# Performance work log

Hardware: AMD Instinct MI355X
Metric: run time of the kernel (lower is better)

Reference implementation:

```python
import jax, jax.numpy as jnp
import numpy as np

N_EMBD = 1024
HEAD_SIZE = 64
TOP_K = 32


def setup_inputs() -> dict:
    key = jax.random.key(0)
    ks = jax.random.split(key, 10)
    B, T, C, D, N = 4, 2048, N_EMBD, HEAD_SIZE, 16384
    s = 1.0 / np.sqrt(C)
    return {
        "x": jax.random.normal(ks[0], (B, T, C), jnp.float32),
        "mem_keys": jax.random.normal(ks[1], (B, N, D), jnp.float32),
        "mem_vals": jax.random.normal(ks[2], (B, N, D), jnp.float32),
        "Wq": jax.random.normal(ks[3], (C, D), jnp.float32) * s,
        "bq": jnp.zeros((D,), jnp.float32),
        "Wk": jax.random.normal(ks[4], (C, D), jnp.float32) * s,
        "bk": jnp.zeros((D,), jnp.float32),
        "Wv": jax.random.normal(ks[5], (C, D), jnp.float32) * s,
        "bv": jnp.zeros((D,), jnp.float32),
        "gate": jax.random.normal(ks[6], (1,), jnp.float32),
    }


def reference(x, mem_keys, mem_vals, Wq, bq, Wk, bk, Wv, bv, gate):
    B, T, C = x.shape
    scale = 1.0 / jnp.sqrt(jnp.asarray(C, x.dtype))  # note: scaled by n_embd, as in source
    q = x @ Wq + bq  # [B,T,D]
    k = x @ Wk + bk
    v = x @ Wv + bv
    # causal self-attention
    att = jnp.einsum("btd,bsd->bts", q, k) * scale
    causal = jnp.tril(jnp.ones((T, T), bool))
    att = jnp.where(causal[None], att, -jnp.inf)
    att = jax.nn.softmax(att, axis=-1)
    out = jnp.einsum("bts,bsd->btd", att, v)  # [B,T,D]
    # kNN memory attention: top-k inner-product search over memory bank
    scores = jnp.einsum("btd,bnd->btn", q, mem_keys)  # [B,T,N]
    _, idx = jax.lax.top_k(scores, TOP_K)  # [B,T,K]
    mem_k = jnp.take_along_axis(mem_keys[:, None], idx[..., None], axis=2)  # [B,T,K,D]
    mem_v = jnp.take_along_axis(mem_vals[:, None], idx[..., None], axis=2)  # [B,T,K,D]
    mem_att = jax.nn.softmax(jnp.einsum("btd,btkd->btk", q, mem_k) * scale, axis=-1)
    mem_out = jnp.einsum("btk,btkd->btd", mem_att, mem_v)  # [B,T,D]
    g = gate[0]
    md_out = out * g + mem_out * (1.0 - g)  # gated combine; dropout is identity at eval
    return md_out
```

## Files before the change

kernel.cpp:

```cpp
#include <hip/hip_runtime.h>
#include <math.h>

#define B_ 4
#define T_ 2048
#define C_ 1024
#define D_ 64
#define N_ 16384
#define K_ 32
#define SCALE 0.03125f
#define NEGINF -3.402823e38f

typedef __attribute__((ext_vector_type(8))) short short8_t;
typedef __attribute__((ext_vector_type(4))) float f32x4;

__device__ __forceinline__ unsigned short f2bf(float x) {
    union { float f; unsigned u; } a; a.f = x;
    const unsigned r = a.u + 0x7fffu + ((a.u >> 16) & 1u);
    return (unsigned short)(r >> 16);
}
__device__ __forceinline__ float bf2f(unsigned short h) {
    union { unsigned u; float f; } a; a.u = ((unsigned)h) << 16;
    return a.f;
}

__global__ __launch_bounds__(192) void qkv_proj_kernel(
    const float* __restrict__ x,
    const float* __restrict__ Wq, const float* __restrict__ bq,
    const float* __restrict__ Wk, const float* __restrict__ bk,
    const float* __restrict__ Wv, const float* __restrict__ bvp,
    float* __restrict__ q, float* __restrict__ k, float* __restrict__ v)
{
    __shared__ float xs[8][C_];
    const int tid = threadIdx.x;
    const int row0 = blockIdx.x * 8;
    const float* xr = x + (size_t)row0 * C_;
    for (int i = tid; i < 8 * C_ / 4; i += 192)
        ((float4*)&xs[0][0])[i] = ((const float4*)xr)[i];
    __syncthreads();
    const int g = tid >> 6;
    const int d = tid & 63;
    const float* W    = (g == 0) ? Wq : (g == 1) ? Wk : Wv;
    const float* bias = (g == 0) ? bq : (g == 1) ? bk : bvp;
    float*       o    = (g == 0) ? q  : (g == 1) ? k  : v;
    float acc[8];
    const float b0 = bias[d];
    #pragma unroll
    for (int r = 0; r < 8; ++r) acc[r] = b0;
    #pragma unroll 4
    for (int c = 0; c < C_; ++c) {
        const float wv = W[c * D_ + d];
        #pragma unroll
        for (int r = 0; r < 8; ++r) acc[r] += xs[r][c] * wv;
    }
    #pragma unroll
    for (int r = 0; r < 8; ++r)
        o[(size_t)(row0 + r) * D_ + d] = acc[r];
}

__global__ __launch_bounds__(256) void kfrag_prep_kernel(
    const float* __restrict__ keys, unsigned short* __restrict__ khi,
    unsigned short* __restrict__ klo)
{
    const int tid = threadIdx.x;
    const int lane = tid & 63;
    const int ks = (tid >> 6) & 1;
    const int b  = blockIdx.x >> 9;
    const int nt = ((blockIdx.x & 511) << 1) | (tid >> 7);
    const int key = nt * 16 + (lane & 15);
    const float* src = keys + ((size_t)b * N_ + key) * D_ + ks * 32 + (lane >> 4) * 8;
    const size_t o = (((size_t)b * 1024 + nt) * 2 + ks) * 512 + (size_t)lane * 8;
    #pragma unroll
    for (int j = 0; j < 8; ++j) {
        const float xv = src[j];
        const unsigned short h = f2bf(xv);
        khi[o + j] = h;
        klo[o + j] = f2bf(xv - bf2f(h));
    }
}

__global__ __launch_bounds__(256) void causal_prep_kernel(
    const float* __restrict__ k, const float* __restrict__ v,
    unsigned short* __restrict__ kcfrag, unsigned short* __restrict__ vfrag)
{
    __shared__ float vtile[64][68];
    const int tid = threadIdx.x;
    const int b = blockIdx.x >> 5;
    const int n64 = blockIdx.x & 31;
    const int w = tid >> 6, lane = tid & 63;
    const int q16 = lane & 15, g = lane >> 4;

    const float4* in4 = (const float4*)(v + ((size_t)b * T_ + n64 * 64) * D_);
    #pragma unroll
    for (int p = 0; p < 4; ++p) {
        const int fi = tid + p * 256;
        const int row = fi >> 4, c4 = fi & 15;
        *(float4*)&vtile[row][c4 * 4] = in4[fi];
    }

    {
        const int key = (n64 * 4 + w) * 16 + q16;
        #pragma unroll
        for (int ks = 0; ks < 2; ++ks) {
            const float* src = k + ((size_t)b * T_ + key) * D_ + ks * 32 + g * 8;
            const float4 x0 = *(const float4*)(src);
            const float4 x1 = *(const float4*)(src + 4);
            unsigned short* dst = kcfrag
                + ((((size_t)b * 128 + n64 * 4 + w) * 2 + ks) * 512) + (size_t)lane * 8;
            dst[0] = f2bf(x0.x); dst[1] = f2bf(x0.y); dst[2] = f2bf(x0.z); dst[3] = f2bf(x0.w);
            dst[4] = f2bf(x1.x); dst[5] = f2bf(x1.y); dst[6] = f2bf(x1.z); dst[7] = f2bf(x1.w);
        }
    }
    __syncthreads();

    #pragma unroll
    for (int ks = 0; ks < 2; ++ks) {
        unsigned short* dst = vfrag
            + ((((size_t)b * 32 + n64) * 8 + ks * 4 + w) * 512) + (size_t)lane * 8;
        #pragma unroll
        for (int j = 0; j < 8; ++j)
            dst[j] = f2bf(vtile[ks * 32 + g * 8 + j][w * 16 + q16]);
    }
}

__global__ __launch_bounds__(256) void causal_flash_kernel(
    const float* __restrict__ qg,
    const unsigned short* __restrict__ kcfrag, const unsigned short* __restrict__ vfrag,
    float* __restrict__ outc)
{
    __shared__ unsigned int plds[64][36];
    __shared__ float po[4][64][17];
    __shared__ float pml[4][2][16];
    const int tid = threadIdx.x;
    const int w = tid >> 6, lane = tid & 63;
    const int q16 = lane & 15, g = lane >> 4;
    const int b = blockIdx.x >> 7;
    const int qt = blockIdx.x & 127;
    const int t0 = qt * 16;
    const int qglob = t0 + q16;
    const int n64 = (qt >> 2) + 1;

    short8_t qf[2];
    #pragma unroll
    for (int ks = 0; ks < 2; ++ks) {
        const float* src = qg + ((size_t)b * T_ + qglob) * D_ + ks * 32 + g * 8;
        const float4 x0 = *(const float4*)(src);
        const float4 x1 = *(const float4*)(src + 4);
        qf[ks][0] = (short)f2bf(x0.x); qf[ks][1] = (short)f2bf(x0.y);
        qf[ks][2] = (short)f2bf(x0.z); qf[ks][3] = (short)f2bf(x0.w);
        qf[ks][4] = (short)f2bf(x1.x); qf[ks][5] = (short)f2bf(x1.y);
        qf[ks][6] = (short)f2bf(x1.z); qf[ks][7] = (short)f2bf(x1.w);
    }

    float m = -1.0e30f, l = 0.f;
    f32x4 o[4];
    #pragma unroll
    for (int dt = 0; dt < 4; ++dt) o[dt] = (f32x4){0.f, 0.f, 0.f, 0.f};

    const int qrow = w * 16 + q16;

    for (int n = w; n < n64; n += 4) {
        short8_t kf[4][2];
        #pragma unroll
        for (int a = 0; a < 4; ++a)
            #pragma unroll
            for (int ks = 0; ks < 2; ++ks)
                kf[a][ks] = *(const short8_t*)(kcfrag
                    + ((((size_t)b * 128 + n * 4 + a) * 2 + ks) * 512) + (size_t)lane * 8);
        f32x4 st[4];
        #pragma unroll
        for (int a = 0; a < 4; ++a) {
            st[a] = (f32x4){0.f, 0.f, 0.f, 0.f};
            st[a] = __builtin_amdgcn_mfma_f32_16x16x32_bf16(kf[a][0], qf[0], st[a], 0, 0, 0);
            st[a] = __builtin_amdgcn_mfma_f32_16x16x32_bf16(kf[a][1], qf[1], st[a], 0, 0, 0);
        }

        float sv[4][4];
        float pm = -1.0e30f;
        #pragma unroll
        for (int a = 0; a < 4; ++a)
            #pragma unroll
            for (int r = 0; r < 4; ++r) {
                const int kk = n * 64 + a * 16 + g * 4 + r;
                float x = st[a][r] * SCALE;
                x = (kk <= qglob) ? x : -1.0e31f;
                sv[a][r] = x;
                pm = fmaxf(pm, x);
            }
        pm = fmaxf(pm, __shfl_xor(pm, 16));
        pm = fmaxf(pm, __shfl_xor(pm, 32));
        const float mn = fmaxf(m, pm);
        const float al = __expf(m - mn);
        float rs = 0.f;
        float ev[4][4];
        #pragma unroll
        for (int a = 0; a < 4; ++a)
            #pragma unroll
            for (int r = 0; r < 4; ++r) {
                const float e = __expf(sv[a][r] - mn);
                ev[a][r] = e;
                rs += e;
            }
        rs += __shfl_xor(rs, 16);
        rs += __shfl_xor(rs, 32);
        l = l * al + rs;
        m = mn;
        #pragma unroll
        for (int dt = 0; dt < 4; ++dt) o[dt] *= al;

        #pragma unroll
        for (int a = 0; a < 4; ++a)
            #pragma unroll
            for (int rp = 0; rp < 2; ++rp)
                plds[qrow][a * 8 + g * 2 + rp] =
                    (unsigned)f2bf(ev[a][2 * rp]) | ((unsigned)f2bf(ev[a][2 * rp + 1]) << 16);
        #pragma unroll
        for (int ks = 0; ks < 2; ++ks) {
            const short8_t pf = *(const short8_t*)&plds[qrow][ks * 16 + g * 4];
            #pragma unroll
            for (int dt = 0; dt < 4; ++dt) {
                const short8_t vf = *(const short8_t*)(vfrag
                    + ((((size_t)b * 32 + n) * 8 + ks * 4 + dt) * 512) + (size_t)lane * 8);
                o[dt] = __builtin_amdgcn_mfma_f32_16x16x32_bf16(vf, pf, o[dt], 0, 0, 0);
            }
        }
    }

    #pragma unroll
    for (int dt = 0; dt < 4; ++dt)
        #pragma unroll
        for (int r = 0; r < 4; ++r)
            po[w][dt * 16 + g * 4 + r][q16] = o[dt][r];
    if (g == 0) { pml[w][0][q16] = m; pml[w][1][q16] = l; }
    __syncthreads();

    {
        const int q = tid & 15;
        const int dgrp = tid >> 4;
        float mw[4], lw[4];
        #pragma unroll
        for (int ww = 0; ww < 4; ++ww) { mw[ww] = pml[ww][0][q]; lw[ww] = pml[ww][1][q]; }
        const float M = fmaxf(fmaxf(mw[0], mw[1]), fmaxf(mw[2], mw[3]));
        float wgt[4], L = 0.f;
        #pragma unroll
        for (int ww = 0; ww < 4; ++ww) {
            wgt[ww] = __expf(mw[ww] - M);
            L += lw[ww] * wgt[ww];
        }
        const float inv = 1.0f / L;
        float4 res;
        float* rp = &res.x;
        #pragma unroll
        for (int i = 0; i < 4; ++i) {
            const int d = dgrp * 4 + i;
            float s = 0.f;
            #pragma unroll
            for (int ww = 0; ww < 4; ++ww) s += po[ww][d][q] * wgt[ww];
            rp[i] = s * inv;
        }
        *(float4*)(outc + ((size_t)b * T_ + t0 + q) * D_ + dgrp * 4) = res;
    }
}

__global__ __launch_bounds__(512) void knn_mfma_kernel(
    const float* __restrict__ qg,
    const unsigned short* __restrict__ khi, const unsigned short* __restrict__ klo,
    const float* __restrict__ mem_vals, const float* __restrict__ outc,
    const float* __restrict__ gate, float* __restrict__ outp)
{
    __shared__ float sc_lds[2][16][260];
    const int tid = threadIdx.x;
    const int w = tid >> 6, lane = tid & 63;
    const int bid = blockIdx.x;
    const int b  = (bid & 7) >> 1;
    const int qt = ((bid >> 3) << 1) | (bid & 1);
    const int t0 = qt * 16;

    short8_t qh[2], ql[2];
    {
        const int qrow = t0 + (lane & 15);
        const float* qs = qg + ((size_t)b * T_ + qrow) * D_ + (lane >> 4) * 8;
        #pragma unroll
        for (int ks2 = 0; ks2 < 2; ++ks2) {
            #pragma unroll
            for (int j = 0; j < 8; ++j) {
                const float xv = qs[ks2 * 32 + j];
                const unsigned short h = f2bf(xv);
                qh[ks2][j] = (short)h;
                ql[ks2][j] = (short)f2bf(xv - bf2f(h));
            }
        }
    }

    const int qrow4 = (lane >> 4) * 4;
    const int c16 = lane & 15;

#define LOADFRAGS(CC, KH, KL)                                                  \
    {                                                                          \
        _Pragma("unroll")                                                      \
        for (int tt = 0; tt < 2; ++tt) {                                       \
            const int tl = w + 8 * tt;                                         \
            const size_t kb = (((size_t)b * 1024 + (size_t)(CC) * 16 + tl) * 2) * 512 \
                            + (size_t)lane * 8;                                \
            KH[tt][0] = *(const short8_t*)(khi + kb);                          \
            KH[tt][1] = *(const short8_t*)(khi + kb + 512);                    \
            KL[tt][0] = *(const short8_t*)(klo + kb);                          \
            KL[tt][1] = *(const short8_t*)(klo + kb + 512);                    \
        }                                                                      \
    }

#define MFMAWRITE(BUF, KH, KL)                                                 \
    {                                                                          \
        _Pragma("unroll")                                                      \
        for (int tt = 0; tt < 2; ++tt) {                                       \
            const int tl = w + 8 * tt;                                         \
            f32x4 acc = {0.f, 0.f, 0.f, 0.f};                                  \
            acc = __builtin_amdgcn_mfma_f32_16x16x32_bf16(qh[0], KH[tt][0], acc, 0, 0, 0); \
            acc = __builtin_amdgcn_mfma_f32_16x16x32_bf16(qh[1], KH[tt][1], acc, 0, 0, 0); \
            acc = __builtin_amdgcn_mfma_f32_16x16x32_bf16(qh[0], KL[tt][0], acc, 0, 0, 0); \
            acc = __builtin_amdgcn_mfma_f32_16x16x32_bf16(qh[1], KL[tt][1], acc, 0, 0, 0); \
            acc = __builtin_amdgcn_mfma_f32_16x16x32_bf16(ql[0], KH[tt][0], acc, 0, 0, 0); \
            acc = __builtin_amdgcn_mfma_f32_16x16x32_bf16(ql[1], KH[tt][1], acc, 0, 0, 0); \
            const int col = tl * 16 + c16;                                     \
            _Pragma("unroll")                                                  \
            for (int r = 0; r < 4; ++r) sc_lds[BUF][qrow4 + r][col] = acc[r];  \
        }                                                                      \
    }

    float rv[2];  int rid_[2];  float t32[2];
    #pragma unroll
    for (int qq = 0; qq < 2; ++qq) {
        rv[qq] = NEGINF; rid_[qq] = 0x7fffffff; t32[qq] = NEGINF;
    }

    {
        short8_t kh[2][2], kl[2][2];
        LOADFRAGS(0, kh, kl);
        MFMAWRITE(0, kh, kl);
    }
    __syncthreads();

    for (int c = 0; c < 64; ++c) {
        short8_t kh[2][2], kl[2][2];
        if (c < 63) LOADFRAGS(c + 1, kh, kl);

        float s4[2][4];
        #pragma unroll
        for (int qq = 0; qq < 2; ++qq)
            *(float4*)(&s4[qq][0]) = *(const float4*)&sc_lds[c & 1][w * 2 + qq][lane * 4];

        if (c == 0) {
            #pragma unroll
            for (int qq = 0; qq < 2; ++qq) {
                float lmax = NEGINF; int lslot = 0;
                #pragma unroll
                for (int j = 0; j < 4; ++j)
                    if (s4[qq][j] > lmax) { lmax = s4[qq][j]; lslot = j; }
                for (int it = 0; it < 32; ++it) {
                    float wm = lmax;
                    #pragma unroll
                    for (int off = 32; off; off >>= 1)
                        wm = fmaxf(wm, __shfl_xor(wm, off));
                    const unsigned long long bal = __ballot(lmax == wm);
                    const int winner = __ffsll((unsigned long long)bal) - 1;
                    const int wslot  = __shfl(lslot, winner);
                    const int widx   = (winner << 2) + (wslot & 3);
                    const unsigned long long gb = __ballot((lane < K_) && (rv[qq] > wm));
                    const int pos = __popcll(gb);
                    const float sv = __shfl_up(rv[qq], 1);
                    const int   si = __shfl_up(rid_[qq], 1);
                    if (lane > pos)       { rv[qq] = sv; rid_[qq] = si; }
                    else if (lane == pos) { rv[qq] = wm; rid_[qq] = widx; }
                    if (lane == winner) {
                        float nm = NEGINF; int ns = 0;
                        #pragma unroll
                        for (int j = 0; j < 4; ++j) {
                            const float vj = (j == lslot) ? NEGINF : s4[qq][j];
                            s4[qq][j] = vj;
                            if (vj > nm) { nm = vj; ns = j; }
                        }
                        lmax = nm; lslot = ns;
                    }
                }
                t32[qq] = __shfl(rv[qq], 31);
            }
        } else {
            #pragma unroll
            for (int qq = 0; qq < 2; ++qq) {
                #pragma unroll
                for (int j = 0; j < 4; ++j) {
                    unsigned long long bb = __ballot(s4[qq][j] > t32[qq]);
                    while (bb) {
                        const int L = __ffsll(bb) - 1;
                        bb &= bb - 1;
                        const float xv = __shfl(s4[qq][j], L);
                        const int xi = (c << 8) + (L << 2) + j;
                        const unsigned long long gb =
                            __ballot((lane < K_) && (rv[qq] > xv));
                        const int pos = __popcll(gb);
                        const float sv = __shfl_up(rv[qq], 1);
                        const int   si = __shfl_up(rid_[qq], 1);
                        if (lane > pos)       { rv[qq] = sv; rid_[qq] = si; }
                        else if (lane == pos) { rv[qq] = xv; rid_[qq] = xi; }
                    }
                }
                t32[qq] = __shfl(rv[qq], 31);
            }
        }

        if (c < 63) MFMAWRITE((c + 1) & 1, kh, kl);
        __syncthreads();
    }

#undef LOADFRAGS
#undef MFMAWRITE

    const float gv = gate[0];
    const float* vb = mem_vals + (size_t)b * N_ * D_;
    #pragma unroll
    for (int qq = 0; qq < 2; ++qq) {
        const float m = __shfl(rv[qq], 0);
        float wgt = (lane < K_) ? __expf((rv[qq] - m) * SCALE) : 0.f;
        float ssum = wgt;
        #pragma unroll
        for (int off = 32; off; off >>= 1) ssum += __shfl_xor(ssum, off);
        float acc = 0.f;
        for (int i = 0; i < K_; ++i) {
            const float wi = __shfl(wgt, i);
            const int   ii = __shfl(rid_[qq], i);
            acc += wi * vb[(size_t)ii * D_ + lane];
        }
        const size_t o = ((size_t)(b * T_ + t0 + w * 2 + qq)) * D_ + lane;
        outp[o] = outc[o] * gv + (acc / ssum) * (1.f - gv);
    }
}

extern "C" void kernel_launch(void* const* d_in, const int* in_sizes, int n_in,
                              void* d_out, int out_size, void* d_ws, size_t ws_size,
                              hipStream_t stream) {
    const float* x        = (const float*)d_in[0];
    const float* mem_keys = (const float*)d_in[1];
    const float* mem_vals = (const float*)d_in[2];
    const float* Wq       = (const float*)d_in[3];
    const float* bq       = (const float*)d_in[4];
    const float* Wk       = (const float*)d_in[5];
    const float* bk       = (const float*)d_in[6];
    const float* Wv       = (const float*)d_in[7];
    const float* bv       = (const float*)d_in[8];
    const float* gate     = (const float*)d_in[9];
    float* out = (float*)d_out;

    const size_t btd = (size_t)B_ * T_ * D_;
    float* q    = (float*)d_ws;
    float* k    = q + btd;
    float* v    = k + btd;
    float* outc = v + btd;
    unsigned short* khi    = (unsigned short*)(outc + btd);
    unsigned short* klo    = khi + (size_t)B_ * N_ * D_;
    unsigned short* kcfrag = klo + (size_t)B_ * N_ * D_;
    unsigned short* vfrag  = kcfrag + btd;

    qkv_proj_kernel<<<B_ * T_ / 8, 192, 0, stream>>>(x, Wq, bq, Wk, bk, Wv, bv, q, k, v);
    kfrag_prep_kernel<<<B_ * 512, 256, 0, stream>>>(mem_keys, khi, klo);
    causal_prep_kernel<<<B_ * 32, 256, 0, stream>>>(k, v, kcfrag, vfrag);
    causal_flash_kernel<<<B_ * 128, 256, 0, stream>>>(q, kcfrag, vfrag, outc);
    knn_mfma_kernel<<<512, 512, 0, stream>>>(q, khi, klo, mem_vals, outc, gate, out);
}
```

Before: 295.5 us.

## Use 16 waves per kNN block, one query row and key tile per wave

The kNN top-k kernel now runs 1024-thread blocks. Each of 16 waves handles one 16-key tile in the MFMA score phase and one query row in the top-k selection, where before 8 waves each handled two. This halves the serial per-wave selection and scoring work and adds more waves to hide latency. In exchange there are more waves per block contending at each __syncthreads, and register pressure may rise under the 1024-thread launch bound.

```diff
diff --git a/kernel.cpp b/kernel.cpp
--- a/kernel.cpp
+++ b/kernel.cpp
@@ -261,7 +261,7 @@
     }
 }
 
-__global__ __launch_bounds__(512) void knn_mfma_kernel(
+__global__ __launch_bounds__(1024) void knn_mfma_kernel(
     const float* __restrict__ qg,
     const unsigned short* __restrict__ khi, const unsigned short* __restrict__ klo,
     const float* __restrict__ mem_vals, const float* __restrict__ outc,
@@ -296,115 +296,94 @@
 
 #define LOADFRAGS(CC, KH, KL)                                                  \
     {                                                                          \
-        _Pragma("unroll")                                                      \
-        for (int tt = 0; tt < 2; ++tt) {                                       \
-            const int tl = w + 8 * tt;                                         \
-            const size_t kb = (((size_t)b * 1024 + (size_t)(CC) * 16 + tl) * 2) * 512 \
-                            + (size_t)lane * 8;                                \
-            KH[tt][0] = *(const short8_t*)(khi + kb);                          \
-            KH[tt][1] = *(const short8_t*)(khi + kb + 512);                    \
-            KL[tt][0] = *(const short8_t*)(klo + kb);                          \
-            KL[tt][1] = *(const short8_t*)(klo + kb + 512);                    \
-        }                                                                      \
+        const size_t kb = (((size_t)b * 1024 + (size_t)(CC) * 16 + w) * 2) * 512 \
+                        + (size_t)lane * 8;                                    \
+        KH[0] = *(const short8_t*)(khi + kb);                                  \
+        KH[1] = *(const short8_t*)(khi + kb + 512);                            \
+        KL[0] = *(const short8_t*)(klo + kb);                                  \
+        KL[1] = *(const short8_t*)(klo + kb + 512);                            \
     }
 
 #define MFMAWRITE(BUF, KH, KL)                                                 \
     {                                                                          \
+        f32x4 acc = {0.f, 0.f, 0.f, 0.f};                                      \
+        acc = __builtin_amdgcn_mfma_f32_16x16x32_bf16(qh[0], KH[0], acc, 0, 0, 0); \
+        acc = __builtin_amdgcn_mfma_f32_16x16x32_bf16(qh[1], KH[1], acc, 0, 0, 0); \
+        acc = __builtin_amdgcn_mfma_f32_16x16x32_bf16(qh[0], KL[0], acc, 0, 0, 0); \
+        acc = __builtin_amdgcn_mfma_f32_16x16x32_bf16(qh[1], KL[1], acc, 0, 0, 0); \
+        acc = __builtin_amdgcn_mfma_f32_16x16x32_bf16(ql[0], KH[0], acc, 0, 0, 0); \
+        acc = __builtin_amdgcn_mfma_f32_16x16x32_bf16(ql[1], KH[1], acc, 0, 0, 0); \
+        const int col = w * 16 + c16;                                          \
         _Pragma("unroll")                                                      \
-        for (int tt = 0; tt < 2; ++tt) {                                       \
-            const int tl = w + 8 * tt;                                         \
-            f32x4 acc = {0.f, 0.f, 0.f, 0.f};                                  \
-            acc = __builtin_amdgcn_mfma_f32_16x16x32_bf16(qh[0], KH[tt][0], acc, 0, 0, 0); \
-            acc = __builtin_amdgcn_mfma_f32_16x16x32_bf16(qh[1], KH[tt][1], acc, 0, 0, 0); \
-            acc = __builtin_amdgcn_mfma_f32_16x16x32_bf16(qh[0], KL[tt][0], acc, 0, 0, 0); \
-            acc = __builtin_amdgcn_mfma_f32_16x16x32_bf16(qh[1], KL[tt][1], acc, 0, 0, 0); \
-            acc = __builtin_amdgcn_mfma_f32_16x16x32_bf16(ql[0], KH[tt][0], acc, 0, 0, 0); \
-            acc = __builtin_amdgcn_mfma_f32_16x16x32_bf16(ql[1], KH[tt][1], acc, 0, 0, 0); \
-            const int col = tl * 16 + c16;                                     \
-            _Pragma("unroll")                                                  \
-            for (int r = 0; r < 4; ++r) sc_lds[BUF][qrow4 + r][col] = acc[r];  \
-        }                                                                      \
-    }
-
-    float rv[2];  int rid_[2];  float t32[2];
-    #pragma unroll
-    for (int qq = 0; qq < 2; ++qq) {
-        rv[qq] = NEGINF; rid_[qq] = 0x7fffffff; t32[qq] = NEGINF;
-    }
+        for (int r = 0; r < 4; ++r) sc_lds[BUF][qrow4 + r][col] = acc[r];      \
+    }
+
+    float rv = NEGINF;  int rid_ = 0x7fffffff;  float t32 = NEGINF;
 
     {
-        short8_t kh[2][2], kl[2][2];
+        short8_t kh[2], kl[2];
         LOADFRAGS(0, kh, kl);
         MFMAWRITE(0, kh, kl);
     }
     __syncthreads();
 
     for (int c = 0; c < 64; ++c) {
-        short8_t kh[2][2], kl[2][2];
+        short8_t kh[2], kl[2];
         if (c < 63) LOADFRAGS(c + 1, kh, kl);
 
-        float s4[2][4];
-        #pragma unroll
-        for (int qq = 0; qq < 2; ++qq)
-            *(float4*)(&s4[qq][0]) = *(const float4*)&sc_lds[c & 1][w * 2 + qq][lane * 4];
+        float s4[4];
+        *(float4*)(&s4[0]) = *(const float4*)&sc_lds[c & 1][w][lane * 4];
 
         if (c == 0) {
-            #pragma unroll
-            for (int qq = 0; qq < 2; ++qq) {
-                float lmax = NEGINF; int lslot = 0;
+            float lmax = NEGINF; int lslot = 0;
+            #pragma unroll
+            for (int j = 0; j < 4; ++j)
+                if (s4[j] > lmax) { lmax = s4[j]; lslot = j; }
+            for (int it = 0; it < 32; ++it) {
+                float wm = lmax;
                 #pragma unroll
-                for (int j = 0; j < 4; ++j)
-                    if (s4[qq][j] > lmax) { lmax = s4[qq][j]; lslot = j; }
-                for (int it = 0; it < 32; ++it) {
-                    float wm = lmax;
+                for (int off = 32; off; off >>= 1)
+                    wm = fmaxf(wm, __shfl_xor(wm, off));
+                const unsigned long long bal = __ballot(lmax == wm);
+                const int winner = __ffsll((unsigned long long)bal) - 1;
+                const int wslot  = __shfl(lslot, winner);
+                const int widx   = (winner << 2) + (wslot & 3);
+                const unsigned long long gb = __ballot((lane < K_) && (rv > wm));
+                const int pos = __popcll(gb);
+                const float sv = __shfl_up(rv, 1);
+                const int   si = __shfl_up(rid_, 1);
+                if (lane > pos)       { rv = sv; rid_ = si; }
+                else if (lane == pos) { rv = wm; rid_ = widx; }
+                if (lane == winner) {
+                    float nm = NEGINF; int ns = 0;
                     #pragma unroll
-                    for (int off = 32; off; off >>= 1)
-                        wm = fmaxf(wm, __shfl_xor(wm, off));
-                    const unsigned long long bal = __ballot(lmax == wm);
-                    const int winner = __ffsll((unsigned long long)bal) - 1;
-                    const int wslot  = __shfl(lslot, winner);
-                    const int widx   = (winner << 2) + (wslot & 3);
-                    const unsigned long long gb = __ballot((lane < K_) && (rv[qq] > wm));
+                    for (int j = 0; j < 4; ++j) {
+                        const float vj = (j == lslot) ? NEGINF : s4[j];
+                        s4[j] = vj;
+                        if (vj > nm) { nm = vj; ns = j; }
+                    }
+                    lmax = nm; lslot = ns;
+                }
+            }
+            t32 = __shfl(rv, 31);
+        } else {
+            #pragma unroll
+            for (int j = 0; j < 4; ++j) {
+                unsigned long long bb = __ballot(s4[j] > t32);
+                while (bb) {
+                    const int L = __ffsll(bb) - 1;
+                    bb &= bb - 1;
+                    const float xv = __shfl(s4[j], L);
+                    const int xi = (c << 8) + (L << 2) + j;
+                    const unsigned long long gb = __ballot((lane < K_) && (rv > xv));
                     const int pos = __popcll(gb);
-                    const float sv = __shfl_up(rv[qq], 1);
-                    const int   si = __shfl_up(rid_[qq], 1);
-                    if (lane > pos)       { rv[qq] = sv; rid_[qq] = si; }
-                    else if (lane == pos) { rv[qq] = wm; rid_[qq] = widx; }
-                    if (lane == winner) {
-                        float nm = NEGINF; int ns = 0;
-                        #pragma unroll
-                        for (int j = 0; j < 4; ++j) {
-                            const float vj = (j == lslot) ? NEGINF : s4[qq][j];
-                            s4[qq][j] = vj;
-                            if (vj > nm) { nm = vj; ns = j; }
-                        }
-                        lmax = nm; lslot = ns;
-                    }
+                    const float sv = __shfl_up(rv, 1);
+                    const int   si = __shfl_up(rid_, 1);
+                    if (lane > pos)       { rv = sv; rid_ = si; }
+                    else if (lane == pos) { rv = xv; rid_ = xi; }
                 }
-                t32[qq] = __shfl(rv[qq], 31);
-            }
-        } else {
-            #pragma unroll
-            for (int qq = 0; qq < 2; ++qq) {
-                #pragma unroll
-                for (int j = 0; j < 4; ++j) {
-                    unsigned long long bb = __ballot(s4[qq][j] > t32[qq]);
-                    while (bb) {
-                        const int L = __ffsll(bb) - 1;
-                        bb &= bb - 1;
-                        const float xv = __shfl(s4[qq][j], L);
-                        const int xi = (c << 8) + (L << 2) + j;
-                        const unsigned long long gb =
-                            __ballot((lane < K_) && (rv[qq] > xv));
-                        const int pos = __popcll(gb);
-                        const float sv = __shfl_up(rv[qq], 1);
-                        const int   si = __shfl_up(rid_[qq], 1);
-                        if (lane > pos)       { rv[qq] = sv; rid_[qq] = si; }
-                        else if (lane == pos) { rv[qq] = xv; rid_[qq] = xi; }
-                    }
-                }
-                t32[qq] = __shfl(rv[qq], 31);
-            }
+            }
+            t32 = __shfl(rv, 31);
         }
 
         if (c < 63) MFMAWRITE((c + 1) & 1, kh, kl);
@@ -416,20 +395,19 @@
 
     const float gv = gate[0];
     const float* vb = mem_vals + (size_t)b * N_ * D_;
-    #pragma unroll
-    for (int qq = 0; qq < 2; ++qq) {
-        const float m = __shfl(rv[qq], 0);
-        float wgt = (lane < K_) ? __expf((rv[qq] - m) * SCALE) : 0.f;
+    {
+        const float m = __shfl(rv, 0);
+        float wgt = (lane < K_) ? __expf((rv - m) * SCALE) : 0.f;
         float ssum = wgt;
         #pragma unroll
         for (int off = 32; off; off >>= 1) ssum += __shfl_xor(ssum, off);
         float acc = 0.f;
         for (int i = 0; i < K_; ++i) {
             const float wi = __shfl(wgt, i);
-            const int   ii = __shfl(rid_[qq], i);
+            const int   ii = __shfl(rid_, i);
             acc += wi * vb[(size_t)ii * D_ + lane];
         }
-        const size_t o = ((size_t)(b * T_ + t0 + w * 2 + qq)) * D_ + lane;
+        const size_t o = ((size_t)(b * T_ + t0 + w)) * D_ + lane;
         outp[o] = outc[o] * gv + (acc / ssum) * (1.f - gv);
     }
 }
@@ -463,5 +441,5 @@
     kfrag_prep_kernel<<<B_ * 512, 256, 0, stream>>>(mem_keys, khi, klo);
     causal_prep_kernel<<<B_ * 32, 256, 0, stream>>>(k, v, kcfrag, vfrag);
     causal_flash_kernel<<<B_ * 128, 256, 0, stream>>>(q, kcfrag, vfrag, outc);
-    knn_mfma_kernel<<<512, 512, 0, stream>>>(q, khi, klo, mem_vals, outc, gate, out);
-}
+    knn_mfma_kernel<<<512, 1024, 0, stream>>>(q, khi, klo, mem_vals, outc, gate, out);
+}
```

Result: slower. 307.4 us (+4.0%).

## Replace scalar QKV projection with split-bf16 MFMA kernel and pre-fragmented weights

Applied to the files above, without the earlier changes.

Replaces the FP32 scalar-FMA QKV projection with an MFMA kernel. Both x and the weights are split into bf16 hi/lo parts, and three MFMA products are summed to keep near-fp32 accuracy. A new prep kernel rearranges Wq/Wk/Wv into MFMA fragment layout in workspace. Each block computes 32 rows across all 192 output columns. x tiles are staged through shared memory with an on-the-fly bf16 split. The aim is to cut the compute cost of the projection stage, at the price of an extra launch and 3x MFMA work for precision.

```diff
diff --git a/kernel.cpp b/kernel.cpp
--- a/kernel.cpp
+++ b/kernel.cpp
@@ -23,38 +23,96 @@
     return a.f;
 }
 
-__global__ __launch_bounds__(192) void qkv_proj_kernel(
+__global__ __launch_bounds__(256) void wfrag_prep_kernel(
+    const float* __restrict__ Wq, const float* __restrict__ Wk,
+    const float* __restrict__ Wv,
+    unsigned short* __restrict__ whfrag, unsigned short* __restrict__ wlfrag)
+{
+    const int tid = threadIdx.x;
+    const int w = tid >> 6, lane = tid & 63;
+    const int id = blockIdx.x * 4 + w;
+    const int ct = id >> 5, ks = id & 31;
+    const float* W = (ct < 4) ? Wq : (ct < 8) ? Wk : Wv;
+    const int colw = (ct & 3) * 16 + (lane & 15);
+    const int k0 = ks * 32 + (lane >> 4) * 8;
+    unsigned short* dh = whfrag + (size_t)id * 512 + (size_t)lane * 8;
+    unsigned short* dl = wlfrag + (size_t)id * 512 + (size_t)lane * 8;
+    #pragma unroll
+    for (int j = 0; j < 8; ++j) {
+        const float val = W[(size_t)(k0 + j) * D_ + colw];
+        const unsigned short h = f2bf(val);
+        dh[j] = h;
+        dl[j] = f2bf(val - bf2f(h));
+    }
+}
+
+__global__ __launch_bounds__(256) void qkv_mfma_kernel(
     const float* __restrict__ x,
-    const float* __restrict__ Wq, const float* __restrict__ bq,
-    const float* __restrict__ Wk, const float* __restrict__ bk,
-    const float* __restrict__ Wv, const float* __restrict__ bvp,
+    const unsigned short* __restrict__ whfrag, const unsigned short* __restrict__ wlfrag,
+    const float* __restrict__ bq, const float* __restrict__ bk,
+    const float* __restrict__ bv,
     float* __restrict__ q, float* __restrict__ k, float* __restrict__ v)
 {
-    __shared__ float xs[8][C_];
+    __shared__ unsigned short xh[32][136], xl[32][136];
     const int tid = threadIdx.x;
-    const int row0 = blockIdx.x * 8;
-    const float* xr = x + (size_t)row0 * C_;
-    for (int i = tid; i < 8 * C_ / 4; i += 192)
-        ((float4*)&xs[0][0])[i] = ((const float4*)xr)[i];
-    __syncthreads();
-    const int g = tid >> 6;
-    const int d = tid & 63;
-    const float* W    = (g == 0) ? Wq : (g == 1) ? Wk : Wv;
-    const float* bias = (g == 0) ? bq : (g == 1) ? bk : bvp;
-    float*       o    = (g == 0) ? q  : (g == 1) ? k  : v;
-    float acc[8];
-    const float b0 = bias[d];
-    #pragma unroll
-    for (int r = 0; r < 8; ++r) acc[r] = b0;
-    #pragma unroll 4
-    for (int c = 0; c < C_; ++c) {
-        const float wv = W[c * D_ + d];
-        #pragma unroll
-        for (int r = 0; r < 8; ++r) acc[r] += xs[r][c] * wv;
-    }
-    #pragma unroll
-    for (int r = 0; r < 8; ++r)
-        o[(size_t)(row0 + r) * D_ + d] = acc[r];
+    const int w = tid >> 6, lane = tid & 63;
+    const int row0 = blockIdx.x * 32;
+    const int rt = w & 1;
+    const int ct0 = (w >> 1) * 6;
+
+    f32x4 acc[6];
+    #pragma unroll
+    for (int i = 0; i < 6; ++i) {
+        const int ct = ct0 + i;
+        const float* bias = (ct < 4) ? bq : (ct < 8) ? bk : bv;
+        const float bb = bias[(ct & 3) * 16 + (lane & 15)];
+        acc[i] = (f32x4){bb, bb, bb, bb};
+    }
+
+    for (int kc = 0; kc < 8; ++kc) {
+        __syncthreads();
+        #pragma unroll
+        for (int p = 0; p < 4; ++p) {
+            const int fi = tid + p * 256;
+            const int row = fi >> 5, c4 = fi & 31;
+            const float4 xv =
+                *(const float4*)(x + (size_t)(row0 + row) * C_ + kc * 128 + c4 * 4);
+            const unsigned short h0 = f2bf(xv.x), h1 = f2bf(xv.y);
+            const unsigned short h2 = f2bf(xv.z), h3 = f2bf(xv.w);
+            xh[row][c4 * 4 + 0] = h0;  xl[row][c4 * 4 + 0] = f2bf(xv.x - bf2f(h0));
+            xh[row][c4 * 4 + 1] = h1;  xl[row][c4 * 4 + 1] = f2bf(xv.y - bf2f(h1));
+            xh[row][c4 * 4 + 2] = h2;  xl[row][c4 * 4 + 2] = f2bf(xv.z - bf2f(h2));
+            xh[row][c4 * 4 + 3] = h3;  xl[row][c4 * 4 + 3] = f2bf(xv.w - bf2f(h3));
+        }
+        __syncthreads();
+        #pragma unroll
+        for (int ks = 0; ks < 4; ++ks) {
+            const int aoff = ks * 32 + (lane >> 4) * 8;
+            const short8_t ah = *(const short8_t*)&xh[rt * 16 + (lane & 15)][aoff];
+            const short8_t al = *(const short8_t*)&xl[rt * 16 + (lane & 15)][aoff];
+            #pragma unroll
+            for (int i = 0; i < 6; ++i) {
+                const size_t tb = ((size_t)(ct0 + i) * 32 + kc * 4 + ks) * 512
+                                + (size_t)lane * 8;
+                const short8_t wh = *(const short8_t*)(whfrag + tb);
+                const short8_t wl = *(const short8_t*)(wlfrag + tb);
+                acc[i] = __builtin_amdgcn_mfma_f32_16x16x32_bf16(ah, wh, acc[i], 0, 0, 0);
+                acc[i] = __builtin_amdgcn_mfma_f32_16x16x32_bf16(ah, wl, acc[i], 0, 0, 0);
+                acc[i] = __builtin_amdgcn_mfma_f32_16x16x32_bf16(al, wh, acc[i], 0, 0, 0);
+            }
+        }
+    }
+
+    #pragma unroll
+    for (int i = 0; i < 6; ++i) {
+        const int ct = ct0 + i;
+        float* o = (ct < 4) ? q : (ct < 8) ? k : v;
+        const int col = (ct & 3) * 16 + (lane & 15);
+        const int rbase = row0 + rt * 16 + (lane >> 4) * 4;
+        #pragma unroll
+        for (int r = 0; r < 4; ++r)
+            o[(size_t)(rbase + r) * D_ + col] = acc[i][r];
+    }
 }
 
 __global__ __launch_bounds__(256) void kfrag_prep_kernel(
@@ -458,8 +516,12 @@
     unsigned short* klo    = khi + (size_t)B_ * N_ * D_;
     unsigned short* kcfrag = klo + (size_t)B_ * N_ * D_;
     unsigned short* vfrag  = kcfrag + btd;
-
-    qkv_proj_kernel<<<B_ * T_ / 8, 192, 0, stream>>>(x, Wq, bq, Wk, bk, Wv, bv, q, k, v);
+    unsigned short* whfrag = vfrag + btd;
+    unsigned short* wlfrag = whfrag + (size_t)384 * 512;
+
+    wfrag_prep_kernel<<<96, 256, 0, stream>>>(Wq, Wk, Wv, whfrag, wlfrag);
+    qkv_mfma_kernel<<<B_ * T_ / 32, 256, 0, stream>>>(x, whfrag, wlfrag,
+                                                      bq, bk, bv, q, k, v);
     kfrag_prep_kernel<<<B_ * 512, 256, 0, stream>>>(mem_keys, khi, klo);
     causal_prep_kernel<<<B_ * 32, 256, 0, stream>>>(k, v, kcfrag, vfrag);
     causal_flash_kernel<<<B_ * 128, 256, 0, stream>>>(q, kcfrag, vfrag, outc);
```

After: 272.4 us. 7.8% less time.
